# Performance work log

Measured on AMD Instinct MI355X. Metric: run time of the kernel, lower is better.

The kernel has to match this reference:

```python
import jax, jax.numpy as jnp
import numpy as np

HIDDEN = 1024
FFN = 4096
NUM_EXPERTS = 8
TOP_K = 2
BATCH, SEQ = 2, 2048


def setup_inputs() -> dict:
    key = jax.random.key(0)
    ks = jax.random.split(key, 6)
    s_h = 1.0 / np.sqrt(HIDDEN)
    s_f = 1.0 / np.sqrt(FFN)
    return {
        "hidden_states": jax.random.normal(ks[0], (BATCH, SEQ, HIDDEN), jnp.float32),
        "gate_w": jax.random.uniform(ks[1], (HIDDEN, NUM_EXPERTS), jnp.float32, -s_h, s_h),
        "gate_b": jax.random.uniform(ks[2], (NUM_EXPERTS,), jnp.float32, -s_h, s_h),
        "w1": jax.random.uniform(ks[3], (NUM_EXPERTS, HIDDEN, FFN), jnp.float32, -s_h, s_h),
        "w3": jax.random.uniform(ks[4], (NUM_EXPERTS, HIDDEN, FFN), jnp.float32, -s_h, s_h),
        "w2": jax.random.uniform(ks[5], (NUM_EXPERTS, FFN, HIDDEN), jnp.float32, -s_f, s_f),
    }


def reference(hidden_states, gate_w, gate_b, w1, w3, w2):
    B, S, D = hidden_states.shape
    T = B * S
    x = hidden_states.reshape(T, D)

    # Router: softmax in fp32, top-2, renormalize (matches torch source)
    logits = x @ gate_w + gate_b                       # [T, E]
    probs = jax.nn.softmax(logits.astype(jnp.float32), axis=-1)
    top_w, top_idx = jax.lax.top_k(probs, TOP_K)       # [T, 2]
    top_w = top_w / jnp.sum(top_w, axis=-1, keepdims=True)

    # Dense combine weights [T, E]: zero for unselected experts.
    combine = jnp.zeros((T, NUM_EXPERTS), jnp.float32)
    combine = combine.at[jnp.arange(T)[:, None], top_idx].set(top_w)
    combine = combine.astype(x.dtype)

    # Grouped SwiGLU expert MLPs (vectorized over experts, zero-weight tokens
    # contribute nothing after combine).
    h = jax.nn.silu(jnp.einsum('td,edf->tef', x, w1)) * jnp.einsum('td,edf->tef', x, w3)
    out_e = jnp.einsum('tef,efd->ted', h, w2)          # [T, E, D]
    out = jnp.einsum('ted,te->td', out_e, combine)     # weighted combine
    return out.reshape(B, S, D)
```

## Files before the change

kernel.cpp:

```cpp
#include <hip/hip_runtime.h>


#define NTOK 4096
#define HID  1024
#define FFN  4096
#define NE   8
#define TM   128
#define CAP  9216
#define MAXT 72

typedef __bf16 bf16x8 __attribute__((ext_vector_type(8)));
typedef float  f32x4  __attribute__((ext_vector_type(4)));

typedef __attribute__((address_space(3))) unsigned int       lds_uint;
typedef const __attribute__((address_space(1))) unsigned int glob_uint;

__device__ __forceinline__ unsigned short f2bf(float f) {
  union { float f; unsigned u; } v; v.f = f;
  return (unsigned short)((v.u + 0x7FFFu + ((v.u >> 16) & 1u)) >> 16);
}

__device__ __forceinline__ void gload16(const void* g, void* l) {
  __builtin_amdgcn_global_load_lds((glob_uint*)g, (lds_uint*)l, 16, 0, 0);
}

__global__ void k0_zero_cvt(const float* __restrict__ x,
                            unsigned short* __restrict__ xbf,
                            float* __restrict__ out,
                            int* __restrict__ counts) {
  int i = blockIdx.x * 256 + threadIdx.x;
  const float4* x4 = (const float4*)x;
  float4 v = x4[i];
  uint2 p;
  p.x = (unsigned)f2bf(v.x) | ((unsigned)f2bf(v.y) << 16);
  p.y = (unsigned)f2bf(v.z) | ((unsigned)f2bf(v.w) << 16);
  ((uint2*)xbf)[i] = p;
  ((float4*)out)[i] = make_float4(0.f, 0.f, 0.f, 0.f);
  if (i < NE) counts[i] = 0;
}

__global__ __launch_bounds__(256) void k1_transpose(
    const float* __restrict__ s0, unsigned short* __restrict__ d0,
    const float* __restrict__ s1, unsigned short* __restrict__ d1,
    int Rfull, int Cfull, int rg0, int cg0, int RW, int CW) {
  __shared__ unsigned short tile[64 * 72];
  int z = blockIdx.z;
  const float* src = (z < 8 ? s0 : s1) + (size_t)(z & 7) * Rfull * Cfull;
  unsigned short* dst = (z < 8 ? d0 : d1) + (size_t)(z & 7) * RW * CW;
  int c0 = blockIdx.x * 64;
  int r0 = blockIdx.y * 64;
  int t = threadIdx.x;
  int q = t >> 4, p = t & 15;

  const float4* s4 = (const float4*)(src + (size_t)(rg0 + r0 + 4 * q) * Cfull
                                     + cg0 + c0) + p;
  unsigned short v[4][4];
#pragma unroll
  for (int u = 0; u < 4; u++) {
    float4 xv = s4[(size_t)u * (Cfull >> 2)];
    v[u][0] = f2bf(xv.x); v[u][1] = f2bf(xv.y);
    v[u][2] = f2bf(xv.z); v[u][3] = f2bf(xv.w);
  }
#pragma unroll
  for (int j = 0; j < 4; j++) {
    ushort4 w = make_ushort4(v[0][j], v[1][j], v[2][j], v[3][j]);
    *(ushort4*)&tile[(4 * p + j) * 72 + 4 * q] = w;
  }
  __syncthreads();
  int b = t & 7;
#pragma unroll
  for (int vi = 0; vi < 2; vi++) {
    int c = (t >> 3) + 32 * vi;
    uint4 w = *(const uint4*)&tile[c * 72 + 8 * b];
    *(uint4*)(dst + (size_t)(c0 + c) * RW + r0 + 8 * b) = w;
  }
}

__global__ void k2_router(const float* __restrict__ x,
                          const float* __restrict__ gw,
                          const float* __restrict__ gb,
                          int* __restrict__ topi, float* __restrict__ topw,
                          int* __restrict__ counts) {
  int wid = threadIdx.x >> 6, lane = threadIdx.x & 63;
  int t = blockIdx.x * 4 + wid;
  const float4* x4 = (const float4*)(x + (size_t)t * HID);
  const float4* g4 = (const float4*)gw;
  float acc[8];
#pragma unroll
  for (int e = 0; e < 8; e++) acc[e] = 0.f;
#pragma unroll
  for (int i = 0; i < 4; i++) {
    float4 xv = x4[i * 64 + lane];
    int dbase = (i * 64 + lane) * 4;
    float xs[4] = {xv.x, xv.y, xv.z, xv.w};
#pragma unroll
    for (int j = 0; j < 4; j++) {
      float4 ga  = g4[(dbase + j) * 2];
      float4 gbv = g4[(dbase + j) * 2 + 1];
      acc[0] += xs[j] * ga.x;  acc[1] += xs[j] * ga.y;
      acc[2] += xs[j] * ga.z;  acc[3] += xs[j] * ga.w;
      acc[4] += xs[j] * gbv.x; acc[5] += xs[j] * gbv.y;
      acc[6] += xs[j] * gbv.z; acc[7] += xs[j] * gbv.w;
    }
  }
#pragma unroll
  for (int e = 0; e < 8; e++)
#pragma unroll
    for (int m = 1; m < 64; m <<= 1) acc[e] += __shfl_xor(acc[e], m);
  if (lane == 0) {
    float lg[8];
#pragma unroll
    for (int e = 0; e < 8; e++) lg[e] = acc[e] + gb[e];
    int i0 = 0; float m0 = lg[0];
#pragma unroll
    for (int e = 1; e < 8; e++) if (lg[e] > m0) { m0 = lg[e]; i0 = e; }
    int i1 = -1; float m1 = -1e30f;
#pragma unroll
    for (int e = 0; e < 8; e++) if (e != i0 && lg[e] > m1) { m1 = lg[e]; i1 = e; }
    float w0 = 1.f / (1.f + __expf(m1 - m0));
    topi[2 * t] = i0; topi[2 * t + 1] = i1;
    topw[2 * t] = w0; topw[2 * t + 1] = 1.f - w0;
    atomicAdd(&counts[i0], 1);
    atomicAdd(&counts[i1], 1);
  }
}

__global__ void k3_scan(const int* __restrict__ counts, int* offs, int* fill,
                        int* tile_e, int* tile_row,
                        int* sorted_tok, float* sorted_w) {
  if (threadIdx.x == 0) {
    int off = 0, tt = 0;
    for (int e = 0; e < NE; e++) {
      offs[e] = off; fill[e] = 0;
      int nt = (counts[e] + TM - 1) >> 7;
      for (int j = 0; j < nt; j++) { tile_e[tt] = e; tile_row[tt] = off + j * TM; tt++; }
      off += nt * TM;
    }
    for (; tt < MAXT; tt++) { tile_e[tt] = -1; tile_row[tt] = 0; }
  }
  for (int i = threadIdx.x; i < CAP; i += 256) { sorted_tok[i] = 0; sorted_w[i] = 0.f; }
}

__global__ void k4_scatter(const int* __restrict__ topi, const float* __restrict__ topw,
                           const int* __restrict__ offs, int* __restrict__ fill,
                           int* __restrict__ sorted_tok, float* __restrict__ sorted_w) {
  int t = blockIdx.x * 256 + threadIdx.x;
#pragma unroll
  for (int k = 0; k < 2; k++) {
    int e = topi[2 * t + k];
    int p = atomicAdd(&fill[e], 1);
    int s = offs[e] + p;
    sorted_tok[s] = t;
    sorted_w[s]   = topw[2 * t + k];
  }
}


template<int CFC>
__global__ __launch_bounds__(256) void k5_gemm_h(
    const unsigned short* __restrict__ xbf,
    const unsigned short* __restrict__ w1t,
    const unsigned short* __restrict__ w3t,
    unsigned short* __restrict__ h,
    const int* __restrict__ tile_e, const int* __restrict__ tile_row,
    const int* __restrict__ sorted_tok, int FCdyn) {
  const int FC = CFC ? CFC : FCdyn;
  __shared__ unsigned short lsA[128 * 32];
  __shared__ unsigned short lsB1[64 * 32];
  __shared__ unsigned short lsB3[64 * 32];

  int tile = blockIdx.x;
  int e = tile_e[tile];
  if (e < 0) return;
  int row0 = tile_row[tile];
  int n0 = blockIdx.y * 64;
  int tid = threadIdx.x;

  int kc = tid & 3, lr = tid >> 2;
  int g = (kc ^ ((lr >> 1) & 3)) * 8;
  int tok0 = sorted_tok[row0 + lr];
  int tok1 = sorted_tok[row0 + lr + 64];
  const unsigned short* ga0 = xbf + (size_t)tok0 * HID + g;
  const unsigned short* ga1 = xbf + (size_t)tok1 * HID + g;
  const unsigned short* gb1 = w1t + ((size_t)e * FC + n0 + lr) * HID + g;
  const unsigned short* gb3 = w3t + ((size_t)e * FC + n0 + lr) * HID + g;
  unsigned short* la0 = lsA  + tid * 8;
  unsigned short* la1 = lsA  + (256 + tid) * 8;
  unsigned short* lb1 = lsB1 + tid * 8;
  unsigned short* lb3 = lsB3 + tid * 8;

  int wid = tid >> 6, lane = tid & 63, lm = lane & 15, q = lane >> 4;
  int wr = wid >> 1, wc = wid & 1;
  int qs = (q ^ ((lm >> 1) & 3)) * 8;
  const unsigned short* As  = lsA  + (wr * 64 + lm) * 32 + qs;
  const unsigned short* B1s = lsB1 + (wc * 32 + lm) * 32 + qs;
  const unsigned short* B3s = lsB3 + (wc * 32 + lm) * 32 + qs;

  f32x4 acc1[4][2] = {};
  f32x4 acc3[4][2] = {};

#pragma unroll 1
  for (int ks = 0; ks < HID / 32; ks++) {
    __syncthreads();
    int k0 = ks * 32;
    gload16(ga0 + k0, la0);
    gload16(ga1 + k0, la1);
    gload16(gb1 + k0, lb1);
    gload16(gb3 + k0, lb3);
    __syncthreads();
    bf16x8 a[4], b1f[2], b3f[2];
#pragma unroll
    for (int ti = 0; ti < 4; ti++) a[ti] = *(const bf16x8*)(As + ti * 512);
#pragma unroll
    for (int tj = 0; tj < 2; tj++) {
      b1f[tj] = *(const bf16x8*)(B1s + tj * 512);
      b3f[tj] = *(const bf16x8*)(B3s + tj * 512);
    }
#pragma unroll
    for (int ti = 0; ti < 4; ti++)
#pragma unroll
      for (int tj = 0; tj < 2; tj++) {
        acc1[ti][tj] = __builtin_amdgcn_mfma_f32_16x16x32_bf16(a[ti], b1f[tj], acc1[ti][tj], 0, 0, 0);
        acc3[ti][tj] = __builtin_amdgcn_mfma_f32_16x16x32_bf16(a[ti], b3f[tj], acc3[ti][tj], 0, 0, 0);
      }
  }

#pragma unroll
  for (int ti = 0; ti < 4; ti++)
#pragma unroll
    for (int tj = 0; tj < 2; tj++)
#pragma unroll
      for (int r = 0; r < 4; r++) {
        float v1 = acc1[ti][tj][r];
        float v3 = acc3[ti][tj][r];
        float hv = (v1 / (1.f + __expf(-v1))) * v3;
        int grow = row0 + wr * 64 + ti * 16 + q * 4 + r;
        int gcol = n0 + wc * 32 + tj * 16 + lm;
        h[(size_t)grow * FC + gcol] = f2bf(hv);
      }
}

template<int CFC>
__global__ __launch_bounds__(256) void k6_gemm_out(
    const unsigned short* __restrict__ h,
    const unsigned short* __restrict__ w2t,
    float* __restrict__ out,
    const int* __restrict__ tile_e, const int* __restrict__ tile_row,
    const int* __restrict__ sorted_tok, const float* __restrict__ sorted_w,
    int FCdyn) {
  const int FC = CFC ? CFC : FCdyn;
  __shared__ unsigned short lsA[128 * 32];
  __shared__ unsigned short lsB[128 * 32];
  __shared__ int   toks[128];
  __shared__ float wts[128];

  int tile = blockIdx.x;
  int e = tile_e[tile];
  if (e < 0) return;
  int row0 = tile_row[tile];
  int n0 = blockIdx.y * 128;
  int tid = threadIdx.x;

  if (tid < 128) { toks[tid] = sorted_tok[row0 + tid]; wts[tid] = sorted_w[row0 + tid]; }

  int kc = tid & 3, lr = tid >> 2;
  int g = (kc ^ ((lr >> 1) & 3)) * 8;
  const unsigned short* ga0 = h + (size_t)(row0 + lr) * FC + g;
  const unsigned short* ga1 = h + (size_t)(row0 + lr + 64) * FC + g;
  const unsigned short* gb0 = w2t + ((size_t)e * HID + n0 + lr) * FC + g;
  const unsigned short* gb1 = w2t + ((size_t)e * HID + n0 + lr + 64) * FC + g;
  unsigned short* la0 = lsA + tid * 8;
  unsigned short* la1 = lsA + (256 + tid) * 8;
  unsigned short* lb0 = lsB + tid * 8;
  unsigned short* lb1 = lsB + (256 + tid) * 8;

  int wid = tid >> 6, lane = tid & 63, lm = lane & 15, q = lane >> 4;
  int wr = wid >> 1, wc = wid & 1;
  int qs = (q ^ ((lm >> 1) & 3)) * 8;
  const unsigned short* As = lsA + (wr * 64 + lm) * 32 + qs;
  const unsigned short* Bs = lsB + (wc * 64 + lm) * 32 + qs;

  f32x4 acc[4][4] = {};

#pragma unroll 1
  for (int ks = 0; ks < FC / 32; ks++) {
    __syncthreads();
    int k0 = ks * 32;
    gload16(ga0 + k0, la0);
    gload16(ga1 + k0, la1);
    gload16(gb0 + k0, lb0);
    gload16(gb1 + k0, lb1);
    __syncthreads();
    bf16x8 a[4], b[4];
#pragma unroll
    for (int ti = 0; ti < 4; ti++) a[ti] = *(const bf16x8*)(As + ti * 512);
#pragma unroll
    for (int tj = 0; tj < 4; tj++) b[tj] = *(const bf16x8*)(Bs + tj * 512);
#pragma unroll
    for (int ti = 0; ti < 4; ti++)
#pragma unroll
      for (int tj = 0; tj < 4; tj++)
        acc[ti][tj] = __builtin_amdgcn_mfma_f32_16x16x32_bf16(a[ti], b[tj], acc[ti][tj], 0, 0, 0);
  }

#pragma unroll
  for (int ti = 0; ti < 4; ti++)
#pragma unroll
    for (int r = 0; r < 4; r++) {
      int lrow = wr * 64 + ti * 16 + q * 4 + r;
      float wt = wts[lrow];
      if (wt != 0.f) {
        int trow = toks[lrow];
#pragma unroll
        for (int tj = 0; tj < 4; tj++) {
          int gcol = n0 + wc * 64 + tj * 16 + lm;
          atomicAdd(&out[(size_t)trow * HID + gcol], acc[ti][tj][r] * wt);
        }
      }
    }
}

extern "C" void kernel_launch(void* const* d_in, const int* in_sizes, int n_in,
                              void* d_out, int out_size, void* d_ws, size_t ws_size,
                              hipStream_t stream) {
  const float* x  = (const float*)d_in[0];
  const float* gw = (const float*)d_in[1];
  const float* gb = (const float*)d_in[2];
  const float* w1 = (const float*)d_in[3];
  const float* w3 = (const float*)d_in[4];
  const float* w2 = (const float*)d_in[5];
  float* out = (float*)d_out;

  char* ws = (char*)d_ws;
  int*   counts     = (int*)(ws + 0);
  int*   fill       = counts + 8;
  int*   offs       = fill + 8;
  int*   tile_e     = offs + 8;
  int*   tile_row   = tile_e + 80;
  int*   topi       = (int*)(ws + 1024);
  float* topw       = (float*)(ws + 33792);
  int*   sorted_tok = (int*)(ws + 66560);
  float* sorted_w   = (float*)(ws + 103424);
  unsigned short* xbf = (unsigned short*)(ws + 147456);
  const size_t base = 8536064ull;

  int FC = FFN;
  while (FC > 64) {
    size_t W  = (size_t)NE * FC * HID * 2;
    size_t Hb = (size_t)CAP * FC * 2;
    if (base + 3 * W + Hb <= ws_size) break;
    FC >>= 1;
  }
  size_t W = (size_t)NE * FC * HID * 2;
  unsigned short* w1t  = (unsigned short*)(ws + base);
  unsigned short* w3t  = (unsigned short*)(ws + base + W);
  unsigned short* w2t  = (unsigned short*)(ws + base + 2 * W);
  unsigned short* hbuf = (unsigned short*)(ws + base + 3 * W);
  int nc = FFN / FC;

  k0_zero_cvt<<<4096, 256, 0, stream>>>(x, xbf, out, counts);
  k2_router<<<1024, 256, 0, stream>>>(x, gw, gb, topi, topw, counts);
  k3_scan<<<1, 256, 0, stream>>>(counts, offs, fill, tile_e, tile_row, sorted_tok, sorted_w);
  k4_scatter<<<16, 256, 0, stream>>>(topi, topw, offs, fill, sorted_tok, sorted_w);

  for (int c = 0; c < nc; c++) {
    int c0 = c * FC;
    k1_transpose<<<dim3(FC / 64, HID / 64, 16), 256, 0, stream>>>(
        w1, w1t, w3, w3t, HID, FFN, 0, c0, HID, FC);
    k1_transpose<<<dim3(HID / 64, FC / 64, 8), 256, 0, stream>>>(
        w2, w2t, nullptr, nullptr, FFN, HID, c0, 0, FC, HID);
    if (FC == 4096) {
      k5_gemm_h<4096><<<dim3(MAXT, FC / 64), 256, 0, stream>>>(
          xbf, w1t, w3t, hbuf, tile_e, tile_row, sorted_tok, FC);
      k6_gemm_out<4096><<<dim3(MAXT, HID / 128), 256, 0, stream>>>(
          hbuf, w2t, out, tile_e, tile_row, sorted_tok, sorted_w, FC);
    } else if (FC == 2048) {
      k5_gemm_h<2048><<<dim3(MAXT, FC / 64), 256, 0, stream>>>(
          xbf, w1t, w3t, hbuf, tile_e, tile_row, sorted_tok, FC);
      k6_gemm_out<2048><<<dim3(MAXT, HID / 128), 256, 0, stream>>>(
          hbuf, w2t, out, tile_e, tile_row, sorted_tok, sorted_w, FC);
    } else if (FC == 1024) {
      k5_gemm_h<1024><<<dim3(MAXT, FC / 64), 256, 0, stream>>>(
          xbf, w1t, w3t, hbuf, tile_e, tile_row, sorted_tok, FC);
      k6_gemm_out<1024><<<dim3(MAXT, HID / 128), 256, 0, stream>>>(
          hbuf, w2t, out, tile_e, tile_row, sorted_tok, sorted_w, FC);
    } else {
      k5_gemm_h<0><<<dim3(MAXT, FC / 64), 256, 0, stream>>>(
          xbf, w1t, w3t, hbuf, tile_e, tile_row, sorted_tok, FC);
      k6_gemm_out<0><<<dim3(MAXT, HID / 128), 256, 0, stream>>>(
          hbuf, w2t, out, tile_e, tile_row, sorted_tok, sorted_w, FC);
    }
  }
}
```

Measured before the change: 936.4 us.

## Rewrite gate/up GEMM as 256x128 tile double-buffered 8-wave kernel

Replaces the first grouped GEMM (x·w1, x·w3 with SwiGLU) with a 512-thread kernel using 256-row expert tiles, 128-column N tiles, 64-wide K steps and double-buffered dynamic LDS. Global-to-LDS loads for the next K step are interleaved with MFMA phases using fine-grained waitcnt, barriers and setprio. Block IDs are remapped in an XCD-aware way in both GEMMs, and the expert token padding changes to 256-row granularity. The larger tiles cut redundant weight and activation reloads and hide load latency. The cost is a larger 128KB LDS footprint and more padded rows per expert.

```diff
diff --git a/kernel.cpp b/kernel.cpp
--- a/kernel.cpp
+++ b/kernel.cpp
@@ -5,9 +5,10 @@
 #define HID  1024
 #define FFN  4096
 #define NE   8
-#define TM   128
-#define CAP  9216
+#define CAP  10240
 #define MAXT 72
+#define MAXT256 40
+#define NKT5 16
 
 typedef __bf16 bf16x8 __attribute__((ext_vector_type(8)));
 typedef float  f32x4  __attribute__((ext_vector_type(4)));
@@ -126,17 +127,20 @@
 }
 
 __global__ void k3_scan(const int* __restrict__ counts, int* offs, int* fill,
-                        int* tile_e, int* tile_row,
+                        int* t128_e, int* t128_row, int* t256_e, int* t256_row,
                         int* sorted_tok, float* sorted_w) {
   if (threadIdx.x == 0) {
-    int off = 0, tt = 0;
+    int off = 0, t1 = 0, t2 = 0;
     for (int e = 0; e < NE; e++) {
       offs[e] = off; fill[e] = 0;
-      int nt = (counts[e] + TM - 1) >> 7;
-      for (int j = 0; j < nt; j++) { tile_e[tt] = e; tile_row[tt] = off + j * TM; tt++; }
-      off += nt * TM;
-    }
-    for (; tt < MAXT; tt++) { tile_e[tt] = -1; tile_row[tt] = 0; }
+      int nt1 = (counts[e] + 127) >> 7;
+      for (int j = 0; j < nt1; j++) { t128_e[t1] = e; t128_row[t1] = off + j * 128; t1++; }
+      int nt2 = (counts[e] + 255) >> 8;
+      for (int j = 0; j < nt2; j++) { t256_e[t2] = e; t256_row[t2] = off + j * 256; t2++; }
+      off += nt2 * 256;
+    }
+    for (; t1 < MAXT; t1++)    { t128_e[t1] = -1; t128_row[t1] = 0; }
+    for (; t2 < MAXT256; t2++) { t256_e[t2] = -1; t256_row[t2] = 0; }
   }
   for (int i = threadIdx.x; i < CAP; i += 256) { sorted_tok[i] = 0; sorted_w[i] = 0.f; }
 }
@@ -156,86 +160,170 @@
 }
 
 
+#define STG2(SMN, HOFF, S0, S1, KN)                        \
+  do {                                                     \
+    gload16((S0) + (KN), (SMN) + (HOFF) + sd);             \
+    gload16((S1) + (KN), (SMN) + (HOFF) + 4096u + sd);     \
+  } while (0)
+
 template<int CFC>
-__global__ __launch_bounds__(256) void k5_gemm_h(
+__global__ __launch_bounds__(512, 2) void k5_gemm_h8(
     const unsigned short* __restrict__ xbf,
     const unsigned short* __restrict__ w1t,
     const unsigned short* __restrict__ w3t,
     unsigned short* __restrict__ h,
-    const int* __restrict__ tile_e, const int* __restrict__ tile_row,
+    const int* __restrict__ t256_e, const int* __restrict__ t256_row,
     const int* __restrict__ sorted_tok, int FCdyn) {
   const int FC = CFC ? CFC : FCdyn;
-  __shared__ unsigned short lsA[128 * 32];
-  __shared__ unsigned short lsB1[64 * 32];
-  __shared__ unsigned short lsB3[64 * 32];
-
-  int tile = blockIdx.x;
-  int e = tile_e[tile];
+  extern __shared__ unsigned short sm[];
+
+  int nb  = gridDim.x;
+  int bid = blockIdx.x;
+  int nid = (bid & 7) * (nb >> 3) + (bid >> 3);
+  int tile = nid % MAXT256;
+  int nblk = nid / MAXT256;
+
+  int e = t256_e[tile];
   if (e < 0) return;
-  int row0 = tile_row[tile];
-  int n0 = blockIdx.y * 64;
+  int row0 = t256_row[tile];
+  int n0 = nblk * 128;
   int tid = threadIdx.x;
 
-  int kc = tid & 3, lr = tid >> 2;
-  int g = (kc ^ ((lr >> 1) & 3)) * 8;
-  int tok0 = sorted_tok[row0 + lr];
-  int tok1 = sorted_tok[row0 + lr + 64];
-  const unsigned short* ga0 = xbf + (size_t)tok0 * HID + g;
-  const unsigned short* ga1 = xbf + (size_t)tok1 * HID + g;
-  const unsigned short* gb1 = w1t + ((size_t)e * FC + n0 + lr) * HID + g;
-  const unsigned short* gb3 = w3t + ((size_t)e * FC + n0 + lr) * HID + g;
-  unsigned short* la0 = lsA  + tid * 8;
-  unsigned short* la1 = lsA  + (256 + tid) * 8;
-  unsigned short* lb1 = lsB1 + tid * 8;
-  unsigned short* lb3 = lsB3 + tid * 8;
+  int sr = tid >> 3;
+  int cs = ((tid & 7) ^ (sr & 7)) * 8;
+  const unsigned short* pA0 = xbf + (size_t)sorted_tok[row0 +       sr] * HID + cs;
+  const unsigned short* pA1 = xbf + (size_t)sorted_tok[row0 +  64 + sr] * HID + cs;
+  const unsigned short* pA2 = xbf + (size_t)sorted_tok[row0 + 128 + sr] * HID + cs;
+  const unsigned short* pA3 = xbf + (size_t)sorted_tok[row0 + 192 + sr] * HID + cs;
+  size_t rb0 = ((size_t)e * FC + n0 + sr) * HID + cs;
+  size_t rb1 = rb0 + (size_t)64 * HID;
+  const unsigned short* pB10 = w1t + rb0;
+  const unsigned short* pB11 = w1t + rb1;
+  const unsigned short* pB30 = w3t + rb0;
+  const unsigned short* pB31 = w3t + rb1;
+  unsigned sd = (unsigned)tid * 8u;
 
   int wid = tid >> 6, lane = tid & 63, lm = lane & 15, q = lane >> 4;
   int wr = wid >> 1, wc = wid & 1;
-  int qs = (q ^ ((lm >> 1) & 3)) * 8;
-  const unsigned short* As  = lsA  + (wr * 64 + lm) * 32 + qs;
-  const unsigned short* B1s = lsB1 + (wc * 32 + lm) * 32 + qs;
-  const unsigned short* B3s = lsB3 + (wc * 32 + lm) * 32 + qs;
-
-  f32x4 acc1[4][2] = {};
-  f32x4 acc3[4][2] = {};
+  unsigned aOff  = (unsigned)(wr * 64 + lm) * 64u;
+  unsigned b1Off = 16384u + (unsigned)(wc * 64 + lm) * 64u;
+  unsigned b3Off = 24576u + (unsigned)(wc * 64 + lm) * 64u;
+  unsigned px0 = (unsigned)((q ^ (lm & 7)) * 8);
+  unsigned px1 = (unsigned)(((4 + q) ^ (lm & 7)) * 8);
+
+  f32x4 acc1[4][4] = {};
+  f32x4 acc3[4][4] = {};
+  bf16x8 af[4][2], bfr[2][2];
+
+  {
+    unsigned short* smn = sm;
+    STG2(smn, 0u,     pA0,  pA1,  0);
+    STG2(smn, 8192u,  pA2,  pA3,  0);
+    STG2(smn, 16384u, pB10, pB11, 0);
+    STG2(smn, 24576u, pB30, pB31, 0);
+  }
+  asm volatile("s_waitcnt vmcnt(2)" ::: "memory");
+  __builtin_amdgcn_s_barrier();
+  __builtin_amdgcn_sched_barrier(0);
 
 #pragma unroll 1
-  for (int ks = 0; ks < HID / 32; ks++) {
-    __syncthreads();
-    int k0 = ks * 32;
-    gload16(ga0 + k0, la0);
-    gload16(ga1 + k0, la1);
-    gload16(gb1 + k0, lb1);
-    gload16(gb3 + k0, lb3);
-    __syncthreads();
-    bf16x8 a[4], b1f[2], b3f[2];
-#pragma unroll
-    for (int ti = 0; ti < 4; ti++) a[ti] = *(const bf16x8*)(As + ti * 512);
-#pragma unroll
-    for (int tj = 0; tj < 2; tj++) {
-      b1f[tj] = *(const bf16x8*)(B1s + tj * 512);
-      b3f[tj] = *(const bf16x8*)(B3s + tj * 512);
-    }
+  for (int kt = 0; kt < NKT5; kt++) {
+    const unsigned short* smc = sm + ((kt & 1) ? 32768u : 0u);
+    unsigned short*       smn = sm + ((kt & 1) ? 0u : 32768u);
+    int kn = ((kt + 1) & (NKT5 - 1)) * 64;
+
+#pragma unroll
+    for (int ti = 0; ti < 4; ti++) {
+      af[ti][0] = *(const bf16x8*)(smc + aOff + ti * 1024u + px0);
+      af[ti][1] = *(const bf16x8*)(smc + aOff + ti * 1024u + px1);
+    }
+#pragma unroll
+    for (int j = 0; j < 2; j++) {
+      bfr[j][0] = *(const bf16x8*)(smc + b1Off + j * 1024u + px0);
+      bfr[j][1] = *(const bf16x8*)(smc + b1Off + j * 1024u + px1);
+    }
+    STG2(smn, 0u, pA0, pA1, kn);
+    __builtin_amdgcn_s_barrier();
+    __builtin_amdgcn_sched_barrier(0);
+    __builtin_amdgcn_s_setprio(1);
 #pragma unroll
     for (int ti = 0; ti < 4; ti++)
 #pragma unroll
-      for (int tj = 0; tj < 2; tj++) {
-        acc1[ti][tj] = __builtin_amdgcn_mfma_f32_16x16x32_bf16(a[ti], b1f[tj], acc1[ti][tj], 0, 0, 0);
-        acc3[ti][tj] = __builtin_amdgcn_mfma_f32_16x16x32_bf16(a[ti], b3f[tj], acc3[ti][tj], 0, 0, 0);
+      for (int j = 0; j < 2; j++) {
+        acc1[ti][j] = __builtin_amdgcn_mfma_f32_16x16x32_bf16(af[ti][0], bfr[j][0], acc1[ti][j], 0, 0, 0);
+        acc1[ti][j] = __builtin_amdgcn_mfma_f32_16x16x32_bf16(af[ti][1], bfr[j][1], acc1[ti][j], 0, 0, 0);
       }
-  }
+    __builtin_amdgcn_s_setprio(0);
+
+#pragma unroll
+    for (int j = 0; j < 2; j++) {
+      bfr[j][0] = *(const bf16x8*)(smc + b1Off + 2048u + j * 1024u + px0);
+      bfr[j][1] = *(const bf16x8*)(smc + b1Off + 2048u + j * 1024u + px1);
+    }
+    STG2(smn, 8192u, pA2, pA3, kn);
+    asm volatile("s_waitcnt vmcnt(4)" ::: "memory");
+    __builtin_amdgcn_s_barrier();
+    __builtin_amdgcn_sched_barrier(0);
+    __builtin_amdgcn_s_setprio(1);
+#pragma unroll
+    for (int ti = 0; ti < 4; ti++)
+#pragma unroll
+      for (int j = 0; j < 2; j++) {
+        acc1[ti][2 + j] = __builtin_amdgcn_mfma_f32_16x16x32_bf16(af[ti][0], bfr[j][0], acc1[ti][2 + j], 0, 0, 0);
+        acc1[ti][2 + j] = __builtin_amdgcn_mfma_f32_16x16x32_bf16(af[ti][1], bfr[j][1], acc1[ti][2 + j], 0, 0, 0);
+      }
+    __builtin_amdgcn_s_setprio(0);
+
+#pragma unroll
+    for (int j = 0; j < 2; j++) {
+      bfr[j][0] = *(const bf16x8*)(smc + b3Off + j * 1024u + px0);
+      bfr[j][1] = *(const bf16x8*)(smc + b3Off + j * 1024u + px1);
+    }
+    STG2(smn, 16384u, pB10, pB11, kn);
+    __builtin_amdgcn_s_barrier();
+    __builtin_amdgcn_sched_barrier(0);
+    __builtin_amdgcn_s_setprio(1);
+#pragma unroll
+    for (int ti = 0; ti < 4; ti++)
+#pragma unroll
+      for (int j = 0; j < 2; j++) {
+        acc3[ti][j] = __builtin_amdgcn_mfma_f32_16x16x32_bf16(af[ti][0], bfr[j][0], acc3[ti][j], 0, 0, 0);
+        acc3[ti][j] = __builtin_amdgcn_mfma_f32_16x16x32_bf16(af[ti][1], bfr[j][1], acc3[ti][j], 0, 0, 0);
+      }
+    __builtin_amdgcn_s_setprio(0);
+
+#pragma unroll
+    for (int j = 0; j < 2; j++) {
+      bfr[j][0] = *(const bf16x8*)(smc + b3Off + 2048u + j * 1024u + px0);
+      bfr[j][1] = *(const bf16x8*)(smc + b3Off + 2048u + j * 1024u + px1);
+    }
+    STG2(smn, 24576u, pB30, pB31, kn);
+    asm volatile("s_waitcnt vmcnt(2)" ::: "memory");
+    __builtin_amdgcn_s_barrier();
+    __builtin_amdgcn_sched_barrier(0);
+    __builtin_amdgcn_s_setprio(1);
+#pragma unroll
+    for (int ti = 0; ti < 4; ti++)
+#pragma unroll
+      for (int j = 0; j < 2; j++) {
+        acc3[ti][2 + j] = __builtin_amdgcn_mfma_f32_16x16x32_bf16(af[ti][0], bfr[j][0], acc3[ti][2 + j], 0, 0, 0);
+        acc3[ti][2 + j] = __builtin_amdgcn_mfma_f32_16x16x32_bf16(af[ti][1], bfr[j][1], acc3[ti][2 + j], 0, 0, 0);
+      }
+    __builtin_amdgcn_s_setprio(0);
+  }
+  asm volatile("s_waitcnt vmcnt(0)" ::: "memory");
 
 #pragma unroll
   for (int ti = 0; ti < 4; ti++)
 #pragma unroll
-    for (int tj = 0; tj < 2; tj++)
+    for (int tj = 0; tj < 4; tj++)
 #pragma unroll
       for (int r = 0; r < 4; r++) {
         float v1 = acc1[ti][tj][r];
         float v3 = acc3[ti][tj][r];
         float hv = (v1 / (1.f + __expf(-v1))) * v3;
         int grow = row0 + wr * 64 + ti * 16 + q * 4 + r;
-        int gcol = n0 + wc * 32 + tj * 16 + lm;
+        int gcol = n0 + wc * 64 + tj * 16 + lm;
         h[(size_t)grow * FC + gcol] = f2bf(hv);
       }
 }
@@ -254,11 +342,16 @@
   __shared__ int   toks[128];
   __shared__ float wts[128];
 
-  int tile = blockIdx.x;
+  int nbk  = (int)(gridDim.x * gridDim.y);
+  int bidl = (int)(blockIdx.x + gridDim.x * blockIdx.y);
+  int nidk = (bidl & 7) * (nbk >> 3) + (bidl >> 3);
+  int tile = nidk % (int)gridDim.x;
+  int yb   = nidk / (int)gridDim.x;
+
   int e = tile_e[tile];
   if (e < 0) return;
   int row0 = tile_row[tile];
-  int n0 = blockIdx.y * 128;
+  int n0 = yb * 128;
   int tid = threadIdx.x;
 
   if (tid < 128) { toks[tid] = sorted_tok[row0 + tid]; wts[tid] = sorted_w[row0 + tid]; }
@@ -333,19 +426,21 @@
 
   char* ws = (char*)d_ws;
   int*   counts     = (int*)(ws + 0);
-  int*   fill       = counts + 8;
-  int*   offs       = fill + 8;
-  int*   tile_e     = offs + 8;
-  int*   tile_row   = tile_e + 80;
-  int*   topi       = (int*)(ws + 1024);
-  float* topw       = (float*)(ws + 33792);
-  int*   sorted_tok = (int*)(ws + 66560);
-  float* sorted_w   = (float*)(ws + 103424);
-  unsigned short* xbf = (unsigned short*)(ws + 147456);
-  const size_t base = 8536064ull;
+  int*   fill       = (int*)(ws + 32);
+  int*   offs       = (int*)(ws + 64);
+  int*   t128_e     = (int*)(ws + 96);
+  int*   t128_row   = (int*)(ws + 416);
+  int*   t256_e     = (int*)(ws + 736);
+  int*   t256_row   = (int*)(ws + 896);
+  int*   topi       = (int*)(ws + 2048);
+  float* topw       = (float*)(ws + 34816);
+  int*   sorted_tok = (int*)(ws + 67584);
+  float* sorted_w   = (float*)(ws + 108544);
+  unsigned short* xbf = (unsigned short*)(ws + 149504);
+  const size_t base = 8538112ull;
 
   int FC = FFN;
-  while (FC > 64) {
+  while (FC > 128) {
     size_t W  = (size_t)NE * FC * HID * 2;
     size_t Hb = (size_t)CAP * FC * 2;
     if (base + 3 * W + Hb <= ws_size) break;
@@ -358,9 +453,19 @@
   unsigned short* hbuf = (unsigned short*)(ws + base + 3 * W);
   int nc = FFN / FC;
 
+  static bool attr_set = false;
+  if (!attr_set) {
+    hipFuncSetAttribute((const void*)k5_gemm_h8<4096>, hipFuncAttributeMaxDynamicSharedMemorySize, 131072);
+    hipFuncSetAttribute((const void*)k5_gemm_h8<2048>, hipFuncAttributeMaxDynamicSharedMemorySize, 131072);
+    hipFuncSetAttribute((const void*)k5_gemm_h8<1024>, hipFuncAttributeMaxDynamicSharedMemorySize, 131072);
+    hipFuncSetAttribute((const void*)k5_gemm_h8<0>,    hipFuncAttributeMaxDynamicSharedMemorySize, 131072);
+    attr_set = true;
+  }
+
   k0_zero_cvt<<<4096, 256, 0, stream>>>(x, xbf, out, counts);
   k2_router<<<1024, 256, 0, stream>>>(x, gw, gb, topi, topw, counts);
-  k3_scan<<<1, 256, 0, stream>>>(counts, offs, fill, tile_e, tile_row, sorted_tok, sorted_w);
+  k3_scan<<<1, 256, 0, stream>>>(counts, offs, fill, t128_e, t128_row,
+                                 t256_e, t256_row, sorted_tok, sorted_w);
   k4_scatter<<<16, 256, 0, stream>>>(topi, topw, offs, fill, sorted_tok, sorted_w);
 
   for (int c = 0; c < nc; c++) {
@@ -369,26 +474,27 @@
         w1, w1t, w3, w3t, HID, FFN, 0, c0, HID, FC);
     k1_transpose<<<dim3(HID / 64, FC / 64, 8), 256, 0, stream>>>(
         w2, w2t, nullptr, nullptr, FFN, HID, c0, 0, FC, HID);
+    dim3 g5(MAXT256 * (FC / 128));
     if (FC == 4096) {
-      k5_gemm_h<4096><<<dim3(MAXT, FC / 64), 256, 0, stream>>>(
-          xbf, w1t, w3t, hbuf, tile_e, tile_row, sorted_tok, FC);
+      k5_gemm_h8<4096><<<g5, 512, 131072, stream>>>(
+          xbf, w1t, w3t, hbuf, t256_e, t256_row, sorted_tok, FC);
       k6_gemm_out<4096><<<dim3(MAXT, HID / 128), 256, 0, stream>>>(
-          hbuf, w2t, out, tile_e, tile_row, sorted_tok, sorted_w, FC);
+          hbuf, w2t, out, t128_e, t128_row, sorted_tok, sorted_w, FC);
     } else if (FC == 2048) {
-      k5_gemm_h<2048><<<dim3(MAXT, FC / 64), 256, 0, stream>>>(
-          xbf, w1t, w3t, hbuf, tile_e, tile_row, sorted_tok, FC);
+      k5_gemm_h8<2048><<<g5, 512, 131072, stream>>>(
+          xbf, w1t, w3t, hbuf, t256_e, t256_row, sorted_tok, FC);
       k6_gemm_out<2048><<<dim3(MAXT, HID / 128), 256, 0, stream>>>(
-          hbuf, w2t, out, tile_e, tile_row, sorted_tok, sorted_w, FC);
+          hbuf, w2t, out, t128_e, t128_row, sorted_tok, sorted_w, FC);
     } else if (FC == 1024) {
-      k5_gemm_h<1024><<<dim3(MAXT, FC / 64), 256, 0, stream>>>(
-          xbf, w1t, w3t, hbuf, tile_e, tile_row, sorted_tok, FC);
+      k5_gemm_h8<1024><<<g5, 512, 131072, stream>>>(
+          xbf, w1t, w3t, hbuf, t256_e, t256_row, sorted_tok, FC);
       k6_gemm_out<1024><<<dim3(MAXT, HID / 128), 256, 0, stream>>>(
-          hbuf, w2t, out, tile_e, tile_row, sorted_tok, sorted_w, FC);
+          hbuf, w2t, out, t128_e, t128_row, sorted_tok, sorted_w, FC);
     } else {
-      k5_gemm_h<0><<<dim3(MAXT, FC / 64), 256, 0, stream>>>(
-          xbf, w1t, w3t, hbuf, tile_e, tile_row, sorted_tok, FC);
+      k5_gemm_h8<0><<<g5, 512, 131072, stream>>>(
+          xbf, w1t, w3t, hbuf, t256_e, t256_row, sorted_tok, FC);
       k6_gemm_out<0><<<dim3(MAXT, HID / 128), 256, 0, stream>>>(
-          hbuf, w2t, out, tile_e, tile_row, sorted_tok, sorted_w, FC);
-    }
-  }
-}
+          hbuf, w2t, out, t128_e, t128_row, sorted_tok, sorted_w, FC);
+    }
+  }
+}
```

Result: faster. 871.1 us (-7.0%).
